# Kernel optimization log

Measured on AMD Instinct MI355X. Metric: run time of the kernel, lower is better.

The kernel has to match this reference:

```python
import jax, jax.numpy as jnp
import numpy as np
from math import sqrt

DIM = 2048
NUM_HEADS = 16
HEAD_DIM = DIM // NUM_HEADS
BSZ, SEQ = 2, 2048


def setup_inputs() -> dict:
    key = jax.random.key(0)
    kx, kq, kk, kv, ko = jax.random.split(key, 5)
    x = jax.random.normal(kx, (BSZ, SEQ, DIM), dtype=jnp.float32)
    # causal additive mask, broadcastable to [B, H, S, S]
    neg = jnp.finfo(jnp.float32).min
    mask = jnp.where(jnp.tril(jnp.ones((SEQ, SEQ), dtype=bool)), 0.0, neg)[None, None]
    s = 1.0 / sqrt(DIM)
    Wq = jax.random.normal(kq, (DIM, DIM), dtype=jnp.float32) * s
    Wk = jax.random.normal(kk, (DIM, DIM), dtype=jnp.float32) * s
    Wv = jax.random.normal(kv, (DIM, DIM), dtype=jnp.float32) * s
    Wo = jax.random.normal(ko, (DIM, DIM), dtype=jnp.float32) * s
    return {"x": x, "mask": mask, "Wq": Wq, "Wk": Wk, "Wv": Wv, "Wo": Wo}


def reference(x, mask, Wq, Wk, Wv, Wo):
    b, s, _ = x.shape
    # nn.Linear: y = x @ W.T
    def proj(W):
        return (x @ W.T).reshape(b, s, NUM_HEADS, HEAD_DIM).transpose(0, 2, 1, 3)  # [b,h,s,d]
    q, k, v = proj(Wq), proj(Wk), proj(Wv)
    scores = jnp.einsum('bhqd,bhkd->bhqk', q, k) / sqrt(HEAD_DIM)
    scores = scores + mask
    attn = jax.nn.softmax(scores.astype(jnp.float32), axis=-1).astype(q.dtype)
    out = jnp.einsum('bhqk,bhkd->bhqd', attn, v)
    out = out.transpose(0, 2, 1, 3).reshape(b, s, -1)
    return out @ Wo.T
```

## Files before the change

### kernel.cpp

```cpp
#include <hip/hip_runtime.h>
#include <hip/hip_bf16.h>
#include <stdint.h>

#define DIM 2048
#define NHEADS 16
#define HDIM 128
#define BATCH 2
#define SEQLEN 2048

using bf16x8 = __attribute__((ext_vector_type(8))) __bf16;
using f32x4  = __attribute__((ext_vector_type(4))) float;
typedef unsigned short u16;
typedef unsigned int u32;

__device__ __forceinline__ void cp16(const void* g, void* lds) {
  __builtin_amdgcn_global_load_lds((const __attribute__((address_space(1))) u32*)g,
                                   (__attribute__((address_space(3))) u32*)lds, 16, 0, 0);
}

__device__ __forceinline__ u16 f2b(float f) {
  u32 u = __float_as_uint(f);
  return (u16)((u + 0x7fffu + ((u >> 16) & 1u)) >> 16);
}

__global__ __launch_bounds__(256) void cvt_kernel(
    const float* __restrict__ x,
    const float* __restrict__ Wq, const float* __restrict__ Wk,
    const float* __restrict__ Wv, const float* __restrict__ Wo,
    u16* __restrict__ xb, u16* __restrict__ wqb, u16* __restrict__ wkb,
    u16* __restrict__ wvb, u16* __restrict__ wob)
{
  const size_t Wsz = (size_t)DIM * DIM;
  const float* src; u16* dst;
  switch (blockIdx.y) {
    case 0:  src = x;        dst = xb;        break;
    case 1:  src = x + Wsz;  dst = xb + Wsz;  break;
    case 2:  src = Wq;       dst = wqb;       break;
    case 3:  src = Wk;       dst = wkb;       break;
    case 4:  src = Wv;       dst = wvb;       break;
    default: src = Wo;       dst = wob;       break;
  }
  size_t i = ((size_t)blockIdx.x * 256 + threadIdx.x) * 8;
  float4 a = *(const float4*)(src + i);
  float4 b = *(const float4*)(src + i + 4);
  union { bf16x8 v; u16 s[8]; } u;
  u.s[0] = f2b(a.x); u.s[1] = f2b(a.y); u.s[2] = f2b(a.z); u.s[3] = f2b(a.w);
  u.s[4] = f2b(b.x); u.s[5] = f2b(b.y); u.s[6] = f2b(b.z); u.s[7] = f2b(b.w);
  *(bf16x8*)(dst + i) = u.v;
}

template<int OM>
__device__ __forceinline__ void gemm_body(const u16* __restrict__ A, const u16* __restrict__ B,
                                          void* Cp, u16* As, u16* Bs)
{
  const int tid = threadIdx.x;
  const int w = tid >> 6, l = tid & 63;
  const int wm = w >> 1, wn = w & 1;
  const int quad = l >> 4, ln = l & 15;
  const int bm = blockIdx.y, bn = blockIdx.x;

  f32x4 acc[4][4];
#pragma unroll
  for (int i = 0; i < 4; ++i)
#pragma unroll
    for (int j = 0; j < 4; ++j) acc[i][j] = (f32x4){0.f, 0.f, 0.f, 0.f};

  const u16* Ag = A + (size_t)(bm * 128 + (tid >> 2)) * DIM + (tid & 3) * 8;
  const u16* Bg = B + (size_t)(bn * 128 + (tid >> 2)) * DIM + (tid & 3) * 8;
  u16* AsW = As + w * 512;
  u16* BsW = Bs + w * 512;

  for (int k0 = 0; k0 < DIM; k0 += 32) {
    cp16(Ag + k0, AsW);
    cp16(Ag + k0 + 64 * DIM, AsW + 2048);
    cp16(Bg + k0, BsW);
    cp16(Bg + k0 + 64 * DIM, BsW + 2048);
    __syncthreads();

    bf16x8 af[4], bfr[4];
#pragma unroll
    for (int mi = 0; mi < 4; ++mi)
      af[mi] = *(const bf16x8*)(As + (wm * 64 + mi * 16 + ln) * 32 + quad * 8);
#pragma unroll
    for (int ni = 0; ni < 4; ++ni)
      bfr[ni] = *(const bf16x8*)(Bs + (wn * 64 + ni * 16 + ln) * 32 + quad * 8);
#pragma unroll
    for (int mi = 0; mi < 4; ++mi)
#pragma unroll
      for (int ni = 0; ni < 4; ++ni)
        acc[mi][ni] = __builtin_amdgcn_mfma_f32_16x16x32_bf16(af[mi], bfr[ni], acc[mi][ni], 0, 0, 0);
    __syncthreads();
  }

  if constexpr (OM == 2) {
#pragma unroll
    for (int mi = 0; mi < 4; ++mi)
#pragma unroll
      for (int ni = 0; ni < 4; ++ni) {
        int i0 = bm * 128 + wm * 64 + mi * 16 + quad * 4;
        int jj = bn * 128 + wn * 64 + ni * 16 + ln;
        int b = i0 >> 11, s0 = i0 & 2047, hh = jj >> 7, d = jj & 127;
        ushort4 v4;
        v4.x = f2b(acc[mi][ni][0]); v4.y = f2b(acc[mi][ni][1]);
        v4.z = f2b(acc[mi][ni][2]); v4.w = f2b(acc[mi][ni][3]);
        size_t off = ((size_t)((b * NHEADS + hh) * HDIM + d)) * SEQLEN + s0;
        *(ushort4*)((u16*)Cp + off) = v4;
      }
  } else {
#pragma unroll
    for (int mi = 0; mi < 4; ++mi)
#pragma unroll
      for (int ni = 0; ni < 4; ++ni)
#pragma unroll
        for (int r = 0; r < 4; ++r) {
          int i = bm * 128 + wm * 64 + mi * 16 + quad * 4 + r;
          int jj = bn * 128 + wn * 64 + ni * 16 + ln;
          if constexpr (OM == 1) {
            int b = i >> 11, s = i & 2047, hh = jj >> 7, d = jj & 127;
            size_t off = ((size_t)((b * NHEADS + hh) * SEQLEN + s)) * HDIM + d;
            ((u16*)Cp)[off] = f2b(acc[mi][ni][r]);
          } else {
            ((float*)Cp)[(size_t)i * DIM + jj] = acc[mi][ni][r];
          }
        }
  }
}

__global__ __launch_bounds__(256) void qkv_kernel(const u16* __restrict__ xb,
    const u16* __restrict__ Wq, const u16* __restrict__ Wk, const u16* __restrict__ Wv,
    u16* __restrict__ Q, u16* __restrict__ Kk, u16* __restrict__ V)
{
  __shared__ __align__(16) u16 As[128 * 32];
  __shared__ __align__(16) u16 Bs[128 * 32];
  if (blockIdx.z == 0)      gemm_body<1>(xb, Wq, Q, As, Bs);
  else if (blockIdx.z == 1) gemm_body<1>(xb, Wk, Kk, As, Bs);
  else                      gemm_body<2>(xb, Wv, V, As, Bs);
}

__global__ __launch_bounds__(256) void out_kernel(const u16* __restrict__ ctx,
    const u16* __restrict__ Wo, float* __restrict__ out)
{
  __shared__ __align__(16) u16 As[128 * 32];
  __shared__ __align__(16) u16 Bs[128 * 32];
  gemm_body<0>(ctx, Wo, out, As, Bs);
}

__global__ __launch_bounds__(256, 2) void attn_kernel(const u16* __restrict__ Q,
    const u16* __restrict__ K, const u16* __restrict__ VT, u16* __restrict__ ctx)
{
  __shared__ __align__(16) u16 Ks[2][64 * 128];
  __shared__ __align__(16) u16 Vt[2][128 * 64];
  __shared__ __align__(16) u16 Ps[4][32 * 64];

  const int tid = threadIdx.x;
  const int w = tid >> 6, l = tid & 63;
  const int quad = l >> 4, ln = l & 15;

  const int j = blockIdx.x;
  const int b = j >> 8;
  const int kk = j & 255;
  const int h = kk >> 4;
  const int q0 = kk & 15;
  const int qt = b ? (15 - q0) : q0;

  const size_t head_off = (size_t)(b * NHEADS + h) * SEQLEN * HDIM;
  const u16* Qg = Q + head_off + (size_t)qt * 128 * HDIM;
  const u16* Kh = K + head_off;
  const u16* Vh = VT + head_off;

  const int swsrc = (tid * 8) ^ (((tid >> 4) & 7) << 3);
  const int swr = (ln & 7) << 3;

  const int vrow = w * 8 + (l >> 3);
  const int vcol = (((l & 7) ^ (l >> 3)) << 3);

  bf16x8 aq[2][4];
#pragma unroll
  for (int chunk = 0; chunk < 2; ++chunk) {
    u16* base = Ks[0] + w * 512;
    const u16* g = Qg + chunk * 8192 + swsrc;
    cp16(g, base); cp16(g + 2048, base + 2048);
    cp16(g + 4096, base + 4096); cp16(g + 6144, base + 6144);
    __syncthreads();
    if ((w >> 1) == chunk) {
      int rl = (w & 1) * 32;
#pragma unroll
      for (int mi = 0; mi < 2; ++mi)
#pragma unroll
        for (int kb = 0; kb < 4; ++kb)
          aq[mi][kb] = *(const bf16x8*)(Ks[0] + (((rl + mi * 16 + ln) * 128 + kb * 32 + quad * 8) ^ swr));
    }
    __syncthreads();
  }

  float m_run[2][4], l_run[2][4];
  f32x4 o[2][8];
#pragma unroll
  for (int mi = 0; mi < 2; ++mi) {
#pragma unroll
    for (int r = 0; r < 4; ++r) { m_run[mi][r] = -1e30f; l_run[mi][r] = 0.f; }
#pragma unroll
    for (int cb = 0; cb < 8; ++cb) o[mi][cb] = (f32x4){0.f, 0.f, 0.f, 0.f};
  }

  const float c2 = 0.08838834764831845f * 1.4426950408889634f;
  const int NT = 2 * qt + 2;

  {
    u16* kb_ = Ks[0] + w * 512;
    const u16* kg = Kh + swsrc;
    cp16(kg, kb_); cp16(kg + 2048, kb_ + 2048);
    cp16(kg + 4096, kb_ + 4096); cp16(kg + 6144, kb_ + 6144);
    u16* vb_ = Vt[0] + w * 512;
    const u16* vg = Vh + (size_t)vrow * SEQLEN + vcol;
    cp16(vg, vb_); cp16(vg + 32 * SEQLEN, vb_ + 2048);
    cp16(vg + 64 * SEQLEN, vb_ + 4096); cp16(vg + 96 * SEQLEN, vb_ + 6144);
  }

  int cur = 0;
  for (int ct = 0; ct < NT; ++ct) {
    if (ct + 1 < NT) {
      u16* kb_ = Ks[cur ^ 1] + w * 512;
      const u16* kg = Kh + (size_t)(ct + 1) * 64 * HDIM + swsrc;
      cp16(kg, kb_); cp16(kg + 2048, kb_ + 2048);
      cp16(kg + 4096, kb_ + 4096); cp16(kg + 6144, kb_ + 6144);
      u16* vb_ = Vt[cur ^ 1] + w * 512;
      const u16* vg = Vh + (size_t)vrow * SEQLEN + (ct + 1) * 64 + vcol;
      cp16(vg, vb_); cp16(vg + 32 * SEQLEN, vb_ + 2048);
      cp16(vg + 64 * SEQLEN, vb_ + 4096); cp16(vg + 96 * SEQLEN, vb_ + 6144);
      asm volatile("s_waitcnt vmcnt(8)" ::: "memory");
    } else {
      asm volatile("s_waitcnt vmcnt(0)" ::: "memory");
    }
    __builtin_amdgcn_s_barrier();
    __builtin_amdgcn_sched_barrier(0);

    const u16* KsC = Ks[cur];
    const u16* VtC = Vt[cur];
    const bool active = !(ct == NT - 1 && w < 2);

    if (active) {
      f32x4 sc[2][4];
#pragma unroll
      for (int mi = 0; mi < 2; ++mi)
#pragma unroll
        for (int nb = 0; nb < 4; ++nb) sc[mi][nb] = (f32x4){0.f, 0.f, 0.f, 0.f};
#pragma unroll
      for (int kb = 0; kb < 4; ++kb) {
        bf16x8 bk[4];
#pragma unroll
        for (int nb = 0; nb < 4; ++nb)
          bk[nb] = *(const bf16x8*)(KsC + (((nb * 16 + ln) * 128 + kb * 32 + quad * 8) ^ swr));
#pragma unroll
        for (int mi = 0; mi < 2; ++mi)
#pragma unroll
          for (int nb = 0; nb < 4; ++nb)
            sc[mi][nb] = __builtin_amdgcn_mfma_f32_16x16x32_bf16(aq[mi][kb], bk[nb], sc[mi][nb], 0, 0, 0);
      }

      if (ct >= 2 * qt) {
        int dd = (2 * qt - ct) * 64;
#pragma unroll
        for (int mi = 0; mi < 2; ++mi)
#pragma unroll
          for (int nb = 0; nb < 4; ++nb) {
            int col = nb * 16 + ln;
#pragma unroll
            for (int r = 0; r < 4; ++r) {
              int row = w * 32 + mi * 16 + quad * 4 + r;
              if (col > row + dd) sc[mi][nb][r] = -1e30f;
            }
          }
      }

#pragma unroll
      for (int mi = 0; mi < 2; ++mi)
#pragma unroll
        for (int r = 0; r < 4; ++r) {
          float mx = fmaxf(fmaxf(sc[mi][0][r], sc[mi][1][r]), fmaxf(sc[mi][2][r], sc[mi][3][r]));
#pragma unroll
          for (int s = 1; s < 16; s <<= 1) mx = fmaxf(mx, __shfl_xor(mx, s, 64));
          float mnew = fmaxf(m_run[mi][r], mx);
          float sum = 0.f;
          float p[4];
#pragma unroll
          for (int nb = 0; nb < 4; ++nb) {
            p[nb] = exp2f((sc[mi][nb][r] - mnew) * c2);
            sum += p[nb];
          }
#pragma unroll
          for (int s = 1; s < 16; s <<= 1) sum += __shfl_xor(sum, s, 64);
          float alpha = exp2f((m_run[mi][r] - mnew) * c2);
          l_run[mi][r] = l_run[mi][r] * alpha + sum;
          m_run[mi][r] = mnew;
#pragma unroll
          for (int cb = 0; cb < 8; ++cb) o[mi][cb][r] *= alpha;
          int row = mi * 16 + quad * 4 + r;
#pragma unroll
          for (int nb = 0; nb < 4; ++nb)
            Ps[w][(row * 64 + nb * 16 + ln) ^ ((row & 7) << 3)] = f2b(p[nb]);
        }

      __builtin_amdgcn_sched_barrier(0);
      asm volatile("s_waitcnt lgkmcnt(0)" ::: "memory");
      __builtin_amdgcn_sched_barrier(0);

#pragma unroll
      for (int tb = 0; tb < 2; ++tb) {
        bf16x8 ap[2];
#pragma unroll
        for (int mi = 0; mi < 2; ++mi)
          ap[mi] = *(const bf16x8*)(&Ps[w][0] + (((mi * 16 + ln) * 64 + tb * 32 + quad * 8) ^ swr));
#pragma unroll
        for (int cb = 0; cb < 8; ++cb) {
          bf16x8 bv = *(const bf16x8*)(VtC + ((cb * 16 + ln) * 64 + ((tb * 32 + quad * 8) ^ swr)));
#pragma unroll
          for (int mi = 0; mi < 2; ++mi)
            o[mi][cb] = __builtin_amdgcn_mfma_f32_16x16x32_bf16(ap[mi], bv, o[mi][cb], 0, 0, 0);
        }
      }
    }

    __builtin_amdgcn_sched_barrier(0);
    asm volatile("s_waitcnt lgkmcnt(0)" ::: "memory");
    __builtin_amdgcn_s_barrier();
    cur ^= 1;
  }

#pragma unroll
  for (int mi = 0; mi < 2; ++mi)
#pragma unroll
    for (int cb = 0; cb < 8; ++cb)
#pragma unroll
      for (int r = 0; r < 4; ++r) {
        float v = o[mi][cb][r] / l_run[mi][r];
        int srow = qt * 128 + w * 32 + mi * 16 + quad * 4 + r;
        size_t off = ((size_t)(b * SEQLEN + srow)) * DIM + h * HDIM + cb * 16 + ln;
        ctx[off] = f2b(v);
      }
}

extern "C" void kernel_launch(void* const* d_in, const int* in_sizes, int n_in,
                              void* d_out, int out_size, void* d_ws, size_t ws_size,
                              hipStream_t stream) {
  const float* x  = (const float*)d_in[0];
  const float* Wq = (const float*)d_in[2];
  const float* Wk = (const float*)d_in[3];
  const float* Wv = (const float*)d_in[4];
  const float* Wo = (const float*)d_in[5];
  float* out = (float*)d_out;

  const size_t HSZ = (size_t)BATCH * NHEADS * SEQLEN * HDIM;
  const size_t WSZ = (size_t)DIM * DIM;
  u16* Qw  = (u16*)d_out;
  u16* xb  = Qw + HSZ;
  u16* wqb = (u16*)d_ws;
  u16* wkb = wqb + WSZ;
  u16* wvb = wkb + WSZ;
  u16* wob = wvb + WSZ;
  u16* Kw  = wob + WSZ;
  u16* Vw  = Kw + HSZ;
  u16* Cw  = Vw + HSZ;

  cvt_kernel<<<dim3(WSZ / (256 * 8), 6), 256, 0, stream>>>(
      x, Wq, Wk, Wv, Wo, xb, wqb, wkb, wvb, wob);
  qkv_kernel<<<dim3(DIM / 128, (BATCH * SEQLEN) / 128, 3), 256, 0, stream>>>(
      xb, wqb, wkb, wvb, Qw, Kw, Vw);
  attn_kernel<<<dim3(BATCH * NHEADS * (SEQLEN / 128)), 256, 0, stream>>>(Qw, Kw, Vw, Cw);
  out_kernel<<<dim3(DIM / 128, (BATCH * SEQLEN) / 128, 1), 256, 0, stream>>>(Cw, wob, out);
}
```

Before: 448.2 us.

## Compute softmax row sums via MFMA with ones vector and skip rescale when max unchanged

Drops the per-row sum reduction (shuffle butterfly) in the online softmax and instead accumulates the row sum l with an extra MFMA against a ones-column B operand. The sum is computed from the bf16-rounded P values. It also skips the alpha rescale of the output accumulators when no row's maximum grew in the wavefront, using a wave-wide any vote. This adds two MFMAs per tile step and a branch, in exchange for fewer shuffles and exp/multiply ops in the softmax.

```diff
diff --git a/kernel.cpp b/kernel.cpp
--- a/kernel.cpp
+++ b/kernel.cpp
@@ -174,6 +174,11 @@
   const int vrow = w * 8 + (l >> 3);
   const int vcol = (((l & 7) ^ (l >> 3)) << 3);
 
+  union { bf16x8 v; u16 s[8]; } bo;
+#pragma unroll
+  for (int e = 0; e < 8; ++e) bo.s[e] = (ln == 0) ? (u16)0x3F80 : (u16)0;
+  const bf16x8 bones = bo.v;
+
   bf16x8 aq[2][4];
 #pragma unroll
   for (int chunk = 0; chunk < 2; ++chunk) {
@@ -193,14 +198,16 @@
     __syncthreads();
   }
 
-  float m_run[2][4], l_run[2][4];
+  float m_run[2][4];
   f32x4 o[2][8];
+  f32x4 ol[2];
 #pragma unroll
   for (int mi = 0; mi < 2; ++mi) {
 #pragma unroll
-    for (int r = 0; r < 4; ++r) { m_run[mi][r] = -1e30f; l_run[mi][r] = 0.f; }
+    for (int r = 0; r < 4; ++r) m_run[mi][r] = -1e30f;
 #pragma unroll
     for (int cb = 0; cb < 8; ++cb) o[mi][cb] = (f32x4){0.f, 0.f, 0.f, 0.f};
+    ol[mi] = (f32x4){0.f, 0.f, 0.f, 0.f};
   }
 
   const float c2 = 0.08838834764831845f * 1.4426950408889634f;
@@ -273,6 +280,8 @@
           }
       }
 
+      float mxv[2][4];
+      bool grow = false;
 #pragma unroll
       for (int mi = 0; mi < 2; ++mi)
 #pragma unroll
@@ -280,25 +289,33 @@
           float mx = fmaxf(fmaxf(sc[mi][0][r], sc[mi][1][r]), fmaxf(sc[mi][2][r], sc[mi][3][r]));
 #pragma unroll
           for (int s = 1; s < 16; s <<= 1) mx = fmaxf(mx, __shfl_xor(mx, s, 64));
-          float mnew = fmaxf(m_run[mi][r], mx);
-          float sum = 0.f;
-          float p[4];
-#pragma unroll
-          for (int nb = 0; nb < 4; ++nb) {
-            p[nb] = exp2f((sc[mi][nb][r] - mnew) * c2);
-            sum += p[nb];
+          mxv[mi][r] = mx;
+          grow = grow || (mx > m_run[mi][r]);
+        }
+
+      if (__any(grow)) {
+#pragma unroll
+        for (int mi = 0; mi < 2; ++mi)
+#pragma unroll
+          for (int r = 0; r < 4; ++r) {
+            float mnew = fmaxf(m_run[mi][r], mxv[mi][r]);
+            float alpha = exp2f((m_run[mi][r] - mnew) * c2);
+            m_run[mi][r] = mnew;
+#pragma unroll
+            for (int cb = 0; cb < 8; ++cb) o[mi][cb][r] *= alpha;
+            ol[mi][r] *= alpha;
           }
-#pragma unroll
-          for (int s = 1; s < 16; s <<= 1) sum += __shfl_xor(sum, s, 64);
-          float alpha = exp2f((m_run[mi][r] - mnew) * c2);
-          l_run[mi][r] = l_run[mi][r] * alpha + sum;
-          m_run[mi][r] = mnew;
-#pragma unroll
-          for (int cb = 0; cb < 8; ++cb) o[mi][cb][r] *= alpha;
+      }
+
+#pragma unroll
+      for (int mi = 0; mi < 2; ++mi)
+#pragma unroll
+        for (int r = 0; r < 4; ++r) {
           int row = mi * 16 + quad * 4 + r;
 #pragma unroll
           for (int nb = 0; nb < 4; ++nb)
-            Ps[w][(row * 64 + nb * 16 + ln) ^ ((row & 7) << 3)] = f2b(p[nb]);
+            Ps[w][(row * 64 + nb * 16 + ln) ^ ((row & 7) << 3)] =
+                f2b(exp2f((sc[mi][nb][r] - m_run[mi][r]) * c2));
         }
 
       __builtin_amdgcn_sched_barrier(0);
@@ -318,6 +335,9 @@
           for (int mi = 0; mi < 2; ++mi)
             o[mi][cb] = __builtin_amdgcn_mfma_f32_16x16x32_bf16(ap[mi], bv, o[mi][cb], 0, 0, 0);
         }
+#pragma unroll
+        for (int mi = 0; mi < 2; ++mi)
+          ol[mi] = __builtin_amdgcn_mfma_f32_16x16x32_bf16(ap[mi], bones, ol[mi], 0, 0, 0);
       }
     }
 
@@ -327,13 +347,20 @@
     cur ^= 1;
   }
 
+  float lv[2][4];
 #pragma unroll
   for (int mi = 0; mi < 2; ++mi)
 #pragma unroll
+    for (int r = 0; r < 4; ++r)
+      lv[mi][r] = __shfl(ol[mi][r], quad * 16, 64);
+
+#pragma unroll
+  for (int mi = 0; mi < 2; ++mi)
+#pragma unroll
     for (int cb = 0; cb < 8; ++cb)
 #pragma unroll
       for (int r = 0; r < 4; ++r) {
-        float v = o[mi][cb][r] / l_run[mi][r];
+        float v = o[mi][cb][r] / lv[mi][r];
         int srow = qt * 128 + w * 32 + mi * 16 + quad * 4 + r;
         size_t off = ((size_t)(b * SEQLEN + srow)) * DIM + h * HDIM + cb * 16 + ln;
         ctx[off] = f2b(v);
```

After: 428.8 us. 1.05x faster.
